# Kernel optimization log

Hardware: AMD Instinct MI355X
Metric: run time of the kernel (lower is better)

The kernel has to match this reference:

```python
import jax, jax.numpy as jnp
import numpy as np
import math

NUM_HEADS = 16
ROPE_BASE = 10000.0


def _rope_cos_sin(seq_len, head_dim, dtype):
    # Qwen2-style rotary embeddings. The torch source builds cos/sin of width
    # head_dim by concatenating freqs with itself, so the first and second
    # halves are identical; the half-width table below is the equivalent math.
    half = head_dim // 2
    inv_freq = 1.0 / (ROPE_BASE ** (jnp.arange(0, head_dim, 2, dtype=jnp.float32) / head_dim))
    t = jnp.arange(seq_len, dtype=jnp.float32)
    freqs = jnp.einsum('i,j->ij', t, inv_freq)  # [S, half]
    cos = jnp.cos(freqs).astype(dtype)[None, None]  # [1,1,S,half]
    sin = jnp.sin(freqs).astype(dtype)[None, None]
    return cos, sin


def _apply_rope(x, cos, sin):
    # x: [B, H, S, D]; split-half rotation (Qwen2 rotate-half convention)
    half = x.shape[-1] // 2
    x1, x2 = x[..., :half], x[..., half:]
    return jnp.concatenate([x1 * cos - x2 * sin, x2 * cos + x1 * sin], axis=-1)


def setup_inputs() -> dict:
    key = jax.random.key(0)
    ks = jax.random.split(key, 5)
    B, S, H = 2, 2048, 2048
    scale = 1.0 / math.sqrt(H)
    return {
        'hidden_states': jax.random.normal(ks[0], (B, S, H), dtype=jnp.float32),
        'Wq': jax.random.normal(ks[1], (H, H), dtype=jnp.float32) * scale,
        'Wk': jax.random.normal(ks[2], (H, H), dtype=jnp.float32) * scale,
        'Wv': jax.random.normal(ks[3], (H, H), dtype=jnp.float32) * scale,
        'Wo': jax.random.normal(ks[4], (H, H), dtype=jnp.float32) * scale,
    }


def reference(hidden_states, Wq, Wk, Wv, Wo):
    B, S, H = hidden_states.shape
    nh = NUM_HEADS
    hd = H // nh

    def proj(W):
        # nn.Linear: x @ W.T ; then [B,S,H] -> [B,nh,S,hd]
        y = jnp.einsum('bsh,oh->bso', hidden_states, W)
        return y.reshape(B, S, nh, hd).transpose(0, 2, 1, 3)

    q, k, v = proj(Wq), proj(Wk), proj(Wv)

    cos, sin = _rope_cos_sin(S, hd, hidden_states.dtype)
    q = _apply_rope(q, cos, sin)
    k = _apply_rope(k, cos, sin)

    scores = jnp.einsum('bhqd,bhkd->bhqk', q, k) / math.sqrt(hd)
    causal = jnp.triu(jnp.full((S, S), -jnp.inf, dtype=scores.dtype), k=1)
    scores = scores + causal[None, None]
    probs = jax.nn.softmax(scores, axis=-1)

    ctx = jnp.einsum('bhqk,bhkd->bhqd', probs, v)  # [B,nh,S,hd]
    ctx = ctx.transpose(0, 2, 1, 3).reshape(B, S, H)
    out = jnp.einsum('bsh,oh->bso', ctx, Wo)
    return out
```

## Files before the change

kernel.cpp:

```cpp
#include <hip/hip_runtime.h>

#define S_LEN 2048
#define HID   2048
#define NHEAD 16
#define HD    128
#define BSZ   2
#define BS_TOT (BSZ * S_LEN)
#define QKS   4096

typedef __bf16 bf16x8 __attribute__((ext_vector_type(8)));
typedef unsigned short u16x8 __attribute__((ext_vector_type(8)));
typedef unsigned short u16x4 __attribute__((ext_vector_type(4)));
typedef float f32x4 __attribute__((ext_vector_type(4)));

static __device__ __forceinline__ bf16x8 as_bf(u16x8 v) { return __builtin_bit_cast(bf16x8, v); }

static __device__ __forceinline__ unsigned short f2bf(float f) {
  __bf16 h = (__bf16)f;
  return __builtin_bit_cast(unsigned short, h);
}
static __device__ __forceinline__ float bf2f(unsigned short b) {
  unsigned int u = ((unsigned int)b) << 16;
  return __builtin_bit_cast(float, u);
}

static __device__ __forceinline__ void gload_lds16(const unsigned short* g, unsigned short* l) {
  __builtin_amdgcn_global_load_lds((const __attribute__((address_space(1))) unsigned int*)g,
                                   (__attribute__((address_space(3))) unsigned int*)l, 16, 0, 0);
}

__global__ __launch_bounds__(256) void cvt_all(const float* __restrict__ hs,
                                               const float* __restrict__ Wq,
                                               const float* __restrict__ Wk,
                                               const float* __restrict__ Wv,
                                               const float* __restrict__ Wo,
                                               unsigned short* __restrict__ hsb,
                                               unsigned short* __restrict__ wall,
                                               float* __restrict__ ct, float* __restrict__ st) {
  int b = (int)blockIdx.x, tid = (int)threadIdx.x;
  if (b < 8192) {
    int i = b * 256 + tid;
    float4 v = ((const float4*)hs)[i];
    ushort4 o; o.x = f2bf(v.x); o.y = f2bf(v.y); o.z = f2bf(v.z); o.w = f2bf(v.w);
    ((ushort4*)hsb)[i] = o;
  } else if (b < 24576) {
    int t = b - 8192;
    int wsel = t >> 12;
    const float* in = (wsel == 0) ? Wq : (wsel == 1) ? Wk : (wsel == 2) ? Wv : Wo;
    int i = (t & 4095) * 256 + tid;
    float4 v = ((const float4*)in)[i];
    ushort4 o; o.x = f2bf(v.x); o.y = f2bf(v.y); o.z = f2bf(v.z); o.w = f2bf(v.w);
    ((ushort4*)(wall + (size_t)wsel * HID * HID))[i] = o;
  } else {
    int id = (b - 24576) * 256 + tid;
    int tt = id >> 6, d = id & 63;
    float inv = powf(10000.0f, -(float)d * (1.0f / 64.0f));
    float f = (float)tt * inv;
    float sv, cv;
    sincosf(f, &sv, &cv);
    ct[id] = cv; st[id] = sv;
  }
}

__global__ __launch_bounds__(256) void rope_apply_k(unsigned short* __restrict__ qk,
                                                    const float* __restrict__ ct,
                                                    const float* __restrict__ st) {
  int id = blockIdx.x * 256 + threadIdx.x;
  int d4 = (id & 15) * 4;
  int h = (id >> 4) & (NHEAD - 1);
  int m = id >> 8;
  int s = m & (S_LEN - 1);
  float4 c  = *(const float4*)(ct + s * 64 + d4);
  float4 sn = *(const float4*)(st + s * 64 + d4);
  size_t base = (size_t)m * QKS + 2048 + h * HD + d4;
  u16x4 k1 = *(u16x4*)(qk + base), k2 = *(u16x4*)(qk + base + 64);
  u16x4 p1, p2;
  float cc[4] = {c.x, c.y, c.z, c.w}, ss[4] = {sn.x, sn.y, sn.z, sn.w};
#pragma unroll
  for (int j = 0; j < 4; ++j) {
    float ak = bf2f(k1[j]), bk = bf2f(k2[j]);
    p1[j] = f2bf(ak * cc[j] - bk * ss[j]);
    p2[j] = f2bf(bk * cc[j] + ak * ss[j]);
  }
  *(u16x4*)(qk + base) = p1;
  *(u16x4*)(qk + base + 64) = p2;
}

template <typename OutT>
__global__ __launch_bounds__(512, 1) void gemm256(const unsigned short* __restrict__ A,
                                                  const unsigned short* __restrict__ Bw,
                                                  OutT* __restrict__ C, int M, int N, int K) {
  __shared__ __align__(16) unsigned short As[2][256 * 64];
  __shared__ __align__(16) unsigned short Bs[2][256 * 64];
  int x = (int)blockIdx.x;
  int chunk = (int)gridDim.x >> 3;
  int x2 = (x & 7) * chunk + (x >> 3);
  const int nbn = N >> 8;
  int bm = x2 / nbn, bn = x2 % nbn;
  int tid = (int)threadIdx.x;
  int l = tid & 63, lr = l & 15, lg = l >> 4;
  int w = tid >> 6;
  int wm = w >> 2, wn = w & 3;

  int srow = 32 * w + (l >> 3);
  int sslot = (l & 7) ^ ((l >> 3) & 7);
  const unsigned short* gA = A + (size_t)(bm * 256 + srow) * K + sslot * 8;
  const unsigned short* gB = Bw + (size_t)(bn * 256 + srow) * K + sslot * 8;

  int rs7 = lr & 7;

  f32x4 zero = {0.f, 0.f, 0.f, 0.f};
  f32x4 acc[8][4];
#pragma unroll
  for (int mi = 0; mi < 8; ++mi)
#pragma unroll
    for (int ni = 0; ni < 4; ++ni) acc[mi][ni] = zero;

  int nk = K >> 6;

#define STAGE256(buf, kt)                                                       \
  do {                                                                          \
    size_t ko_ = (size_t)(kt) * 64;                                             \
    _Pragma("unroll") for (int i_ = 0; i_ < 4; ++i_) {                          \
      gload_lds16(gA + (size_t)(8 * i_) * K + ko_, &As[buf][(32 * w + 8 * i_) * 64]); \
      gload_lds16(gB + (size_t)(8 * i_) * K + ko_, &Bs[buf][(32 * w + 8 * i_) * 64]); \
    }                                                                           \
  } while (0)

  STAGE256(0, 0);
  __syncthreads();

  for (int kt = 0; kt < nk; ++kt) {
    if (kt + 1 < nk) STAGE256((kt + 1) & 1, kt + 1);
    const unsigned short* Ab = &As[kt & 1][0];
    const unsigned short* Bb = &Bs[kt & 1][0];

    u16x8 bfr[4][2];
#pragma unroll
    for (int ni = 0; ni < 4; ++ni)
#pragma unroll
      for (int ks = 0; ks < 2; ++ks)
        bfr[ni][ks] = *(const u16x8*)&Bb[(wn * 64 + ni * 16 + lr) * 64 + (((ks * 4 + lg) ^ rs7) * 8)];

#pragma unroll
    for (int mq = 0; mq < 4; ++mq) {
      u16x8 af[2][2];
#pragma unroll
      for (int m2 = 0; m2 < 2; ++m2)
#pragma unroll
        for (int ks = 0; ks < 2; ++ks)
          af[m2][ks] = *(const u16x8*)&Ab[(wm * 128 + (2 * mq + m2) * 16 + lr) * 64 + (((ks * 4 + lg) ^ rs7) * 8)];
      __builtin_amdgcn_s_setprio(1);
#pragma unroll
      for (int m2 = 0; m2 < 2; ++m2)
#pragma unroll
        for (int ni = 0; ni < 4; ++ni)
#pragma unroll
          for (int ks = 0; ks < 2; ++ks)
            acc[2 * mq + m2][ni] = __builtin_amdgcn_mfma_f32_16x16x32_bf16(
                as_bf(af[m2][ks]), as_bf(bfr[ni][ks]), acc[2 * mq + m2][ni], 0, 0, 0);
      __builtin_amdgcn_s_setprio(0);
      __builtin_amdgcn_s_barrier();
    }
    __syncthreads();
  }
#undef STAGE256

#pragma unroll
  for (int mi = 0; mi < 8; ++mi) {
#pragma unroll
    for (int ni = 0; ni < 4; ++ni) {
      int col = bn * 256 + wn * 64 + ni * 16 + lr;
#pragma unroll
      for (int j = 0; j < 4; ++j) {
        int rowm = bm * 256 + wm * 128 + mi * 16 + 4 * lg + j;
        float v = acc[mi][ni][j];
        if constexpr (sizeof(OutT) == 2) C[(size_t)rowm * N + col] = f2bf(v);
        else                             C[(size_t)rowm * N + col] = v;
      }
    }
  }
  (void)M;
}

template <typename OutT>
__global__ __launch_bounds__(256) void gemm128(const unsigned short* __restrict__ A,
                                               const unsigned short* __restrict__ Bw,
                                               OutT* __restrict__ C, int M, int N, int K) {
  __shared__ __align__(16) unsigned short As[4][128 * 32];
  __shared__ __align__(16) unsigned short Bs[4][128 * 32];
  int x = (int)blockIdx.x;
  int chunk = (int)gridDim.x >> 3;
  int x2 = (x & 7) * chunk + (x >> 3);
  const int nbn = N >> 7;
  int bm = x2 / nbn, bn = x2 % nbn;
  int tid = (int)threadIdx.x;
  int l = tid & 63, lr = l & 15, lg = l >> 4;
  int w = tid >> 6, wm = w >> 1, wn = w & 1;

  int w32 = 32 * w;
  int srow = w32 + (l >> 2);
  int ssw = ((l >> 2) ^ (l >> 4)) & 3;
  const unsigned short* gA = A + (size_t)(bm * 128 + srow) * K + (((l & 3) ^ ssw) << 3);
  const unsigned short* gB = Bw + (size_t)(bn * 128 + srow) * K + (((l & 3) ^ ssw) << 3);

  int rsw = (lr ^ (lr >> 2)) & 3;
  int aoff[4], boff[4];
#pragma unroll
  for (int i = 0; i < 4; ++i) {
    aoff[i] = (wm * 64 + i * 16 + lr) * 32 + ((lg ^ rsw) << 3);
    boff[i] = (wn * 64 + i * 16 + lr) * 32 + ((lg ^ rsw) << 3);
  }

  f32x4 zero = {0.f, 0.f, 0.f, 0.f};
  f32x4 acc[4][4];
#pragma unroll
  for (int mi = 0; mi < 4; ++mi)
#pragma unroll
    for (int ni = 0; ni < 4; ++ni) acc[mi][ni] = zero;

  int nk = K >> 5;

#define STAGE(buf, kt)                                                        \
  do {                                                                        \
    const unsigned short* pa_ = gA + (size_t)(kt) * 32;                       \
    const unsigned short* pb_ = gB + (size_t)(kt) * 32;                       \
    gload_lds16(pa_, &As[buf][w32 * 32]);                                     \
    gload_lds16(pa_ + (size_t)16 * K, &As[buf][(w32 + 16) * 32]);             \
    gload_lds16(pb_, &Bs[buf][w32 * 32]);                                     \
    gload_lds16(pb_ + (size_t)16 * K, &Bs[buf][(w32 + 16) * 32]);             \
  } while (0)

#define COMPUTE(buf)                                                          \
  do {                                                                        \
    u16x8 af[4], bfr[4];                                                      \
    _Pragma("unroll") for (int i = 0; i < 4; ++i) {                           \
      af[i] = *(const u16x8*)&As[buf][aoff[i]];                               \
      bfr[i] = *(const u16x8*)&Bs[buf][boff[i]];                              \
    }                                                                         \
    _Pragma("unroll") for (int mi = 0; mi < 4; ++mi)                          \
        _Pragma("unroll") for (int ni = 0; ni < 4; ++ni)                      \
            acc[mi][ni] = __builtin_amdgcn_mfma_f32_16x16x32_bf16(            \
                as_bf(af[mi]), as_bf(bfr[ni]), acc[mi][ni], 0, 0, 0);         \
  } while (0)

  STAGE(0, 0);
  STAGE(1, 1);
  STAGE(2, 2);
  asm volatile("s_waitcnt vmcnt(8)" ::: "memory");
  __builtin_amdgcn_s_barrier();
#pragma unroll 4
  for (int kt = 0; kt < nk; ++kt) {
    COMPUTE(kt & 3);
    asm volatile("s_waitcnt vmcnt(4) lgkmcnt(0)" ::: "memory");
    __builtin_amdgcn_s_barrier();
    STAGE((kt + 3) & 3, (kt + 3) & (nk - 1));
  }
#undef STAGE
#undef COMPUTE

#pragma unroll
  for (int mi = 0; mi < 4; ++mi) {
#pragma unroll
    for (int ni = 0; ni < 4; ++ni) {
      int col = bn * 128 + wn * 64 + ni * 16 + lr;
#pragma unroll
      for (int j = 0; j < 4; ++j) {
        int rowm = bm * 128 + wm * 64 + mi * 16 + 4 * lg + j;
        float v = acc[mi][ni][j];
        if constexpr (sizeof(OutT) == 2) C[(size_t)rowm * N + col] = f2bf(v);
        else                             C[(size_t)rowm * N + col] = v;
      }
    }
  }
  (void)M;
}

__global__ __launch_bounds__(256, 2) void attn_fwd(const unsigned short* __restrict__ qk,
                                                   const unsigned short* __restrict__ vt,
                                                   unsigned short* __restrict__ ctx,
                                                   const float* __restrict__ ct,
                                                   const float* __restrict__ st) {
  __shared__ __align__(16) unsigned short Ks[2][64 * 128];
  __shared__ __align__(16) unsigned short Vs[2][128 * 64];
  __shared__ __align__(16) unsigned short Ps[4 * 32 * 64];

  int x = (int)blockIdx.x;
  int bh, qt;
  if (x < 256) { bh = x & 31;         qt = 15 - (x >> 5); }
  else         { bh = (x - 256) & 31; qt = (x - 256) >> 5; }
  int b = bh >> 4, h = bh & 15;
  int q0 = qt * 128;
  int nt = 2 * qt + 2;

  int tid = (int)threadIdx.x;
  int w = tid >> 6, l = tid & 63, lr = l & 15, lg = l >> 4;
  const float CEXP = 0.12751744f;
  const float MB   = -23.0831391f;
  const int bS = b * S_LEN, h128 = h * HD;
  const int qw = q0 + w * 32;
  const unsigned short* qg = qk;
  const unsigned short* kg = qk + 2048;

  u16x8 qfr[2][4];
#pragma unroll
  for (int qf = 0; qf < 2; ++qf) {
    const unsigned short* qb = qg + (size_t)(bS + qw + qf * 16 + lr) * QKS + h128;
#pragma unroll
    for (int kk = 0; kk < 4; ++kk) qfr[qf][kk] = *(const u16x8*)(qb + kk * 32 + lg * 8);
    int spos = qw + qf * 16 + lr;
#pragma unroll
    for (int kk = 0; kk < 2; ++kk) {
      int d0 = kk * 32 + lg * 8;
      float4 c0 = *(const float4*)(ct + spos * 64 + d0);
      float4 c1 = *(const float4*)(ct + spos * 64 + d0 + 4);
      float4 s0 = *(const float4*)(st + spos * 64 + d0);
      float4 s1 = *(const float4*)(st + spos * 64 + d0 + 4);
      float cc[8] = {c0.x, c0.y, c0.z, c0.w, c1.x, c1.y, c1.z, c1.w};
      float sv[8] = {s0.x, s0.y, s0.z, s0.w, s1.x, s1.y, s1.z, s1.w};
      u16x8 lo = qfr[qf][kk], hi = qfr[qf][kk + 2];
#pragma unroll
      for (int j = 0; j < 8; ++j) {
        float a = bf2f(lo[j]), b2 = bf2f(hi[j]);
        lo[j] = f2bf(a * cc[j] - b2 * sv[j]);
        hi[j] = f2bf(b2 * cc[j] + a * sv[j]);
      }
      qfr[qf][kk] = lo; qfr[qf][kk + 2] = hi;
    }
  }

  const unsigned short* kbg[4];
  const unsigned short* vbg[4];
#pragma unroll
  for (int i = 0; i < 4; ++i) {
    int rr = 16 * w + 4 * i + (l >> 4);
    int colK = ((l & 15) ^ (rr & 15)) * 8;
    kbg[i] = kg + (size_t)(bS + rr) * QKS + h128 + colK;
    int vd = 32 * w + 8 * i + (l >> 3);
    int colV = ((l & 7) ^ (vd & 7)) * 8;
    vbg[i] = vt + (size_t)(h128 + vd) * BS_TOT + bS + colV;
  }

#define ASTAGE(buf, t)                                                        \
  do {                                                                        \
    size_t koff_ = (size_t)(t) * 64 * QKS;                                    \
    int voff_ = (t) * 64;                                                     \
    _Pragma("unroll") for (int i_ = 0; i_ < 4; ++i_) {                        \
      gload_lds16(kbg[i_] + koff_, &Ks[buf][(16 * w + 4 * i_) * 128]);        \
      gload_lds16(vbg[i_] + voff_, &Vs[buf][(32 * w + 8 * i_) * 64]);         \
    }                                                                         \
  } while (0)

  f32x4 zero = {0.f, 0.f, 0.f, 0.f};
  f32x4 oacc[2][8];
#pragma unroll
  for (int qf = 0; qf < 2; ++qf)
#pragma unroll
    for (int nj = 0; nj < 8; ++nj) oacc[qf][nj] = zero;
  float lsum[2] = {0.f, 0.f};

  int cur = 0;
  ASTAGE(0, 0);
  __syncthreads();

  for (int t = 0; t < nt; ++t) {
    int k0 = t * 64;
    if (t + 1 < nt) ASTAGE(cur ^ 1, t + 1);

    if (k0 <= qw + 31) {
      const unsigned short* KsB = &Ks[cur][0];
      const unsigned short* VsB = &Vs[cur][0];
      f32x4 sac[2][4];
#pragma unroll
      for (int qf = 0; qf < 2; ++qf)
#pragma unroll
        for (int ni = 0; ni < 4; ++ni) sac[qf][ni] = zero;
      __builtin_amdgcn_s_setprio(1);
#pragma unroll
      for (int kk = 0; kk < 4; ++kk) {
#pragma unroll
        for (int ni = 0; ni < 4; ++ni) {
          u16x8 kf = *(const u16x8*)&KsB[(ni * 16 + lr) * 128 + (((kk * 4 + lg) ^ lr) * 8)];
          sac[0][ni] = __builtin_amdgcn_mfma_f32_16x16x32_bf16(as_bf(kf), as_bf(qfr[0][kk]), sac[0][ni], 0, 0, 0);
          sac[1][ni] = __builtin_amdgcn_mfma_f32_16x16x32_bf16(as_bf(kf), as_bf(qfr[1][kk]), sac[1][ni], 0, 0, 0);
        }
      }
      __builtin_amdgcn_s_setprio(0);
      bool needmask = (k0 + 63 > qw);

#pragma unroll
      for (int qf = 0; qf < 2; ++qf) {
        float s[4][4];
#pragma unroll
        for (int ni = 0; ni < 4; ++ni)
#pragma unroll
          for (int j = 0; j < 4; ++j) s[ni][j] = sac[qf][ni][j];
        if (needmask) {
          int qgl = qw + qf * 16 + lr;
#pragma unroll
          for (int ni = 0; ni < 4; ++ni)
#pragma unroll
            for (int j = 0; j < 4; ++j)
              if (k0 + ni * 16 + 4 * lg + j > qgl) s[ni][j] = -1e30f;
        }
        float rs = 0.f;
#pragma unroll
        for (int ni = 0; ni < 4; ++ni)
#pragma unroll
          for (int j = 0; j < 4; ++j) {
            float p = exp2f(fmaf(s[ni][j], CEXP, MB));
            s[ni][j] = p; rs += p;
          }
        lsum[qf] += rs;
        unsigned short* pw = &Ps[w * 2048];
#pragma unroll
        for (int ni = 0; ni < 4; ++ni) {
          u16x4 pv = {f2bf(s[ni][0]), f2bf(s[ni][1]), f2bf(s[ni][2]), f2bf(s[ni][3])};
          *(u16x4*)&pw[(qf * 16 + lr) * 64 + (((2 * ni + (lg >> 1)) ^ (lr & 7)) * 8) + (lg & 1) * 4] = pv;
        }
      }

      const unsigned short* pw = &Ps[w * 2048];
      __builtin_amdgcn_s_setprio(1);
#pragma unroll
      for (int kk2 = 0; kk2 < 2; ++kk2) {
        u16x8 pa0 = *(const u16x8*)&pw[(0 * 16 + lr) * 64 + (((kk2 * 4 + lg) ^ (lr & 7)) * 8)];
        u16x8 pa1 = *(const u16x8*)&pw[(1 * 16 + lr) * 64 + (((kk2 * 4 + lg) ^ (lr & 7)) * 8)];
#pragma unroll
        for (int nj = 0; nj < 8; ++nj) {
          u16x8 vf = *(const u16x8*)&VsB[(nj * 16 + lr) * 64 + (((kk2 * 4 + lg) ^ (lr & 7)) * 8)];
          oacc[0][nj] = __builtin_amdgcn_mfma_f32_16x16x32_bf16(as_bf(pa0), as_bf(vf), oacc[0][nj], 0, 0, 0);
          oacc[1][nj] = __builtin_amdgcn_mfma_f32_16x16x32_bf16(as_bf(pa1), as_bf(vf), oacc[1][nj], 0, 0, 0);
        }
      }
      __builtin_amdgcn_s_setprio(0);
    }

    __syncthreads();
    cur ^= 1;
  }
#undef ASTAGE

#pragma unroll
  for (int qf = 0; qf < 2; ++qf) {
    float ls = lsum[qf];
    ls += __shfl_xor(ls, 16);
    ls += __shfl_xor(ls, 32);
    float rl = 1.0f / ls;
    float r0 = __shfl(rl, 4 * lg + 0, 16);
    float r1 = __shfl(rl, 4 * lg + 1, 16);
    float r2 = __shfl(rl, 4 * lg + 2, 16);
    float r3 = __shfl(rl, 4 * lg + 3, 16);
    size_t obase = (size_t)(bS + qw + qf * 16 + 4 * lg) * HID + h128;
#pragma unroll
    for (int nj = 0; nj < 8; ++nj) {
      ctx[obase + 0 * HID + nj * 16 + lr] = f2bf(oacc[qf][nj][0] * r0);
      ctx[obase + 1 * HID + nj * 16 + lr] = f2bf(oacc[qf][nj][1] * r1);
      ctx[obase + 2 * HID + nj * 16 + lr] = f2bf(oacc[qf][nj][2] * r2);
      ctx[obase + 3 * HID + nj * 16 + lr] = f2bf(oacc[qf][nj][3] * r3);
    }
  }
}

extern "C" void kernel_launch(void* const* d_in, const int* in_sizes, int n_in,
                              void* d_out, int out_size, void* d_ws, size_t ws_size,
                              hipStream_t stream) {
  const float* hs = (const float*)d_in[0];
  const float* Wq = (const float*)d_in[1];
  const float* Wk = (const float*)d_in[2];
  const float* Wv = (const float*)d_in[3];
  const float* Wo = (const float*)d_in[4];

  char* ws = (char*)d_ws;
  unsigned short* hsb  = (unsigned short*)(ws);
  unsigned short* wall = (unsigned short*)(ws + 16777216);
  unsigned short* qkb  = (unsigned short*)(ws + 50331648);
  unsigned short* vtb  = (unsigned short*)(ws + 83886080);
  float* ctab = (float*)(ws + 100663296);
  float* stab = (float*)(ws + 101187584);
  unsigned short* ctxb = hsb;

  cvt_all<<<25088, 256, 0, stream>>>(hs, Wq, Wk, Wv, Wo, hsb, wall, ctab, stab);

  gemm256<unsigned short><<<256, 512, 0, stream>>>(hsb, wall, qkb, BS_TOT, 2 * HID, HID);
  gemm128<unsigned short><<<512, 256, 0, stream>>>(wall + 2 * (size_t)HID * HID, hsb, vtb, HID, BS_TOT, HID);

  rope_apply_k<<<4096, 256, 0, stream>>>(qkb, ctab, stab);

  attn_fwd<<<512, 256, 0, stream>>>(qkb, vtb, ctxb, ctab, stab);

  gemm128<float><<<512, 256, 0, stream>>>(ctxb, wall + 3 * (size_t)HID * HID, (float*)d_out, BS_TOT, HID, HID);

  (void)in_sizes; (void)n_in; (void)out_size; (void)ws_size;
}
```

Before: 270.8 us.

## Split long causal query tiles across two KV halves with a combine kernel

The attention launch now splits each of the heaviest query tiles (qt 8-15) into two blocks, each covering half of the key range, so the longest blocks take about half as many KV tiles. The short tiles still run unsplit, and the grid grows to 768 blocks to even out per-CU work. Each split block writes a normalized bf16 partial output and its row sum into the freed Wq/Wk/Wv workspace. A new combine kernel then reweights the two partials by their sums into ctx. This cuts the load-imbalance tail but adds an extra kernel launch, extra global traffic for the partials, and one more bf16 rounding step.

```diff
diff --git a/kernel.cpp b/kernel.cpp
--- a/kernel.cpp
+++ b/kernel.cpp
@@ -280,18 +280,35 @@
                                                    const unsigned short* __restrict__ vt,
                                                    unsigned short* __restrict__ ctx,
                                                    const float* __restrict__ ct,
-                                                   const float* __restrict__ st) {
+                                                   const float* __restrict__ st,
+                                                   unsigned short* __restrict__ pO,
+                                                   float* __restrict__ pls) {
   __shared__ __align__(16) unsigned short Ks[2][64 * 128];
   __shared__ __align__(16) unsigned short Vs[2][128 * 64];
   __shared__ __align__(16) unsigned short Ps[4 * 32 * 64];
 
   int x = (int)blockIdx.x;
-  int bh, qt;
-  if (x < 256) { bh = x & 31;         qt = 15 - (x >> 5); }
-  else         { bh = (x - 256) & 31; qt = (x - 256) >> 5; }
+  int bh, qt, half, tile0, ntL;
+  bool split;
+  if (x < 512) {
+    split = true;
+    bh = x & 31;
+    int pair = x >> 5;
+    qt = 15 - (pair >> 1);
+    half = pair & 1;
+    ntL = qt + 1;
+    tile0 = half * ntL;
+  } else {
+    split = false;
+    int i = x - 512;
+    bh = i & 31;
+    qt = 7 - (i >> 5);
+    half = 0;
+    ntL = 2 * qt + 2;
+    tile0 = 0;
+  }
   int b = bh >> 4, h = bh & 15;
   int q0 = qt * 128;
-  int nt = 2 * qt + 2;
 
   int tid = (int)threadIdx.x;
   int w = tid >> 6, l = tid & 63, lr = l & 15, lg = l >> 4;
@@ -360,12 +377,13 @@
   float lsum[2] = {0.f, 0.f};
 
   int cur = 0;
-  ASTAGE(0, 0);
+  ASTAGE(0, tile0);
   __syncthreads();
 
-  for (int t = 0; t < nt; ++t) {
+  for (int tl = 0; tl < ntL; ++tl) {
+    int t = tile0 + tl;
     int k0 = t * 64;
-    if (t + 1 < nt) ASTAGE(cur ^ 1, t + 1);
+    if (tl + 1 < ntL) ASTAGE(cur ^ 1, t + 1);
 
     if (k0 <= qw + 31) {
       const unsigned short* KsB = &Ks[cur][0];
@@ -451,15 +469,51 @@
     float r1 = __shfl(rl, 4 * lg + 1, 16);
     float r2 = __shfl(rl, 4 * lg + 2, 16);
     float r3 = __shfl(rl, 4 * lg + 3, 16);
-    size_t obase = (size_t)(bS + qw + qf * 16 + 4 * lg) * HID + h128;
-#pragma unroll
-    for (int nj = 0; nj < 8; ++nj) {
-      ctx[obase + 0 * HID + nj * 16 + lr] = f2bf(oacc[qf][nj][0] * r0);
-      ctx[obase + 1 * HID + nj * 16 + lr] = f2bf(oacc[qf][nj][1] * r1);
-      ctx[obase + 2 * HID + nj * 16 + lr] = f2bf(oacc[qf][nj][2] * r2);
-      ctx[obase + 3 * HID + nj * 16 + lr] = f2bf(oacc[qf][nj][3] * r3);
+    if (!split) {
+      size_t obase = (size_t)(bS + qw + qf * 16 + 4 * lg) * HID + h128;
+#pragma unroll
+      for (int nj = 0; nj < 8; ++nj) {
+        ctx[obase + 0 * HID + nj * 16 + lr] = f2bf(oacc[qf][nj][0] * r0);
+        ctx[obase + 1 * HID + nj * 16 + lr] = f2bf(oacc[qf][nj][1] * r1);
+        ctx[obase + 2 * HID + nj * 16 + lr] = f2bf(oacc[qf][nj][2] * r2);
+        ctx[obase + 3 * HID + nj * 16 + lr] = f2bf(oacc[qf][nj][3] * r3);
+      }
+    } else {
+      int t256 = (qt - 8) * 32 + bh;
+      int rowq = w * 32 + qf * 16 + 4 * lg;
+      size_t pbase = ((size_t)(half * 256 + t256) * 128 + rowq) * 128;
+#pragma unroll
+      for (int nj = 0; nj < 8; ++nj) {
+        pO[pbase + 0 * 128 + nj * 16 + lr] = f2bf(oacc[qf][nj][0] * r0);
+        pO[pbase + 1 * 128 + nj * 16 + lr] = f2bf(oacc[qf][nj][1] * r1);
+        pO[pbase + 2 * 128 + nj * 16 + lr] = f2bf(oacc[qf][nj][2] * r2);
+        pO[pbase + 3 * 128 + nj * 16 + lr] = f2bf(oacc[qf][nj][3] * r3);
+      }
+      if (lg == 0)
+        pls[(half * 256 + t256) * 128 + w * 32 + qf * 16 + lr] = ls;
     }
   }
+}
+
+__global__ __launch_bounds__(256) void combine(const unsigned short* __restrict__ pO,
+                                               const float* __restrict__ pls,
+                                               unsigned short* __restrict__ ctx) {
+  int vid = blockIdx.x * 256 + threadIdx.x;
+  int t = vid >> 11;
+  int rr = (vid >> 4) & 127;
+  int d8 = vid & 15;
+  int qt8 = t >> 5, bh = t & 31, b = bh >> 4, h = bh & 15;
+  float l1 = pls[t * 128 + rr];
+  float l2 = pls[(256 + t) * 128 + rr];
+  float inv = 1.0f / (l1 + l2);
+  float w1 = l1 * inv, w2 = l2 * inv;
+  u16x8 a = *(const u16x8*)&pO[((size_t)t * 128 + rr) * 128 + d8 * 8];
+  u16x8 c = *(const u16x8*)&pO[((size_t)(256 + t) * 128 + rr) * 128 + d8 * 8];
+  u16x8 o;
+#pragma unroll
+  for (int j = 0; j < 8; ++j) o[j] = f2bf(bf2f(a[j]) * w1 + bf2f(c[j]) * w2);
+  size_t obase = (size_t)(b * S_LEN + (qt8 + 8) * 128 + rr) * HID + h * HD + d8 * 8;
+  *(u16x8*)&ctx[obase] = o;
 }
 
 extern "C" void kernel_launch(void* const* d_in, const int* in_sizes, int n_in,
@@ -479,6 +533,8 @@
   float* ctab = (float*)(ws + 100663296);
   float* stab = (float*)(ws + 101187584);
   unsigned short* ctxb = hsb;
+  unsigned short* pO = wall;
+  float* pls = (float*)(ws + 16777216 + 16777216);
 
   cvt_all<<<25088, 256, 0, stream>>>(hs, Wq, Wk, Wv, Wo, hsb, wall, ctab, stab);
 
@@ -487,7 +543,8 @@
 
   rope_apply_k<<<4096, 256, 0, stream>>>(qkb, ctab, stab);
 
-  attn_fwd<<<512, 256, 0, stream>>>(qkb, vtb, ctxb, ctab, stab);
+  attn_fwd<<<768, 256, 0, stream>>>(qkb, vtb, ctxb, ctab, stab, pO, pls);
+  combine<<<2048, 256, 0, stream>>>(pO, pls, ctxb);
 
   gemm128<float><<<512, 256, 0, stream>>>(ctxb, wall + 3 * (size_t)HID * HID, (float*)d_out, BS_TOT, HID, HID);
 
```

Result: no change. 276.0 us (+1.9%).
